# Optimization experiments

Hardware: AMD Instinct MI355X
Metric: run time of the kernel (lower is better)

## Reference

```python
import jax, jax.numpy as jnp
import numpy as np

B, T, C, H = 16, 2048, 1024, 64

def setup_inputs() -> dict:
    key = jax.random.key(0)
    kx, kq, kk, kv = jax.random.split(key, 4)
    s = 0.02
    return {
        "x": jax.random.normal(kx, (B, T, C), dtype=jnp.float32),
        "Wq": jax.random.normal(kq, (C, H), dtype=jnp.float32) * s,
        "Wk": jax.random.normal(kk, (C, H), dtype=jnp.float32) * s,
        "Wv": jax.random.normal(kv, (C, H), dtype=jnp.float32) * s,
    }

def reference(x, Wq, Wk, Wv):
    Bc, Tc, Cc = x.shape
    q = x @ Wq  # [B,T,H]
    k = x @ Wk  # [B,T,H]
    v = x @ Wv  # [B,T,H]
    # NOTE: original scales by n_embed^{-0.5} (C), not head_size^{-0.5}
    wei = jnp.einsum("bth,bsh->bts", q, k) * (Cc ** -0.5)  # [B,T,T]
    causal = jnp.tril(jnp.ones((Tc, Tc), dtype=bool))
    wei = jnp.where(causal, wei, -jnp.inf)
    wei = jax.nn.softmax(wei, axis=-1)
    # dropout is identity in eval mode
    out = jnp.einsum("bts,bsh->bth", wei, v)  # [B,T,H]
    return out
```

## Files before the change

### kernel.cpp

```cpp
#include <hip/hip_runtime.h>

typedef __attribute__((ext_vector_type(8))) short short8;
typedef __attribute__((ext_vector_type(4))) float float4v;

__device__ inline short f2bf(float f) {
    union { float f; unsigned int u; } c; c.f = f;
    unsigned int u = c.u;
    unsigned int r = (u + 0x7fffu + ((u >> 16) & 1u)) >> 16;
    return (short)r;
}

__device__ inline void gl2lds16(const short* g, short* l) {
    __builtin_amdgcn_global_load_lds(
        (const __attribute__((address_space(1))) unsigned int*)g,
        (__attribute__((address_space(3))) unsigned int*)l, 16, 0, 0);
}


__global__ __launch_bounds__(256) void wconv_kernel(
    const float* __restrict__ Wq, const float* __restrict__ Wk,
    const float* __restrict__ Wv, short* __restrict__ Wt_s)
{
    __shared__ short Ls[64 * 72];
    const int w  = blockIdx.x >> 4;
    const int c  = blockIdx.x & 15;
    const int k0 = c * 64;
    const float* W = (w == 0) ? Wq : (w == 1) ? Wk : Wv;
    const int tid = threadIdx.x;

#pragma unroll
    for (int i = 0; i < 4; i++) {
        int kk = (tid >> 4) + i * 16;
        int c4 = (tid & 15) * 4;
        float4 v = *(const float4*)&W[(size_t)(k0 + kk) * 64 + c4];
        Ls[kk * 72 + c4 + 0] = f2bf(v.x);
        Ls[kk * 72 + c4 + 1] = f2bf(v.y);
        Ls[kk * 72 + c4 + 2] = f2bf(v.z);
        Ls[kk * 72 + c4 + 3] = f2bf(v.w);
    }
    __syncthreads();
    const int n  = tid >> 2;
    const int k8 = (tid & 3) * 16;
    short8 o0, o1;
#pragma unroll
    for (int j = 0; j < 8; j++) o0[j] = Ls[(k8 + j) * 72 + n];
#pragma unroll
    for (int j = 0; j < 8; j++) o1[j] = Ls[(k8 + 8 + j) * 72 + n];
    const int gn = w * 64 + n;
    short* base = &Wt_s[((size_t)c * 192 + gn) * 64];
    int g0 = k8 >> 3;
    *(short8*)&base[((g0    ) ^ (gn & 7)) * 8] = o0;
    *(short8*)&base[((g0 + 1) ^ (gn & 7)) * 8] = o1;
}

__global__ __launch_bounds__(256) void qkv_kernel(
    const float* __restrict__ x, const short* __restrict__ Wt_s,
    short* __restrict__ qo, short* __restrict__ k_s, short* __restrict__ vT_t)
{
    __shared__ short As[32 * 72];
    __shared__ short Bs[192 * 64];

    const int tid  = threadIdx.x;
    const int wave = tid >> 6, lane = tid & 63;
    const int quad = lane >> 4, l16 = lane & 15;
    const int m0   = blockIdx.x * 32;

    float4v acc[2][3];
#pragma unroll
    for (int mf = 0; mf < 2; mf++)
#pragma unroll
        for (int nt = 0; nt < 3; nt++) acc[mf][nt] = (float4v)0.0f;

    const int arow = tid >> 3;
    const int acol = (tid & 7) * 8;
    const float* ap = &x[(size_t)(m0 + arow) * 1024 + acol];
    const int lofs = lane * 8;

    for (int kc = 0; kc < 1024; kc += 64) {
        __syncthreads();
        float4 x0 = *(const float4*)(ap + kc);
        float4 x1 = *(const float4*)(ap + kc + 4);
        short8 av;
        av[0]=f2bf(x0.x); av[1]=f2bf(x0.y); av[2]=f2bf(x0.z); av[3]=f2bf(x0.w);
        av[4]=f2bf(x1.x); av[5]=f2bf(x1.y); av[6]=f2bf(x1.z); av[7]=f2bf(x1.w);
        *(short8*)&As[arow * 72 + acol] = av;
        const short* gsrc = Wt_s + ((size_t)(kc >> 6) * 192 + wave * 48) * 64;
        short* ldst = &Bs[wave * 48 * 64];
#pragma unroll
        for (int i = 0; i < 6; i++)
            gl2lds16(gsrc + i * 512 + lofs, ldst + i * 512 + lofs);
        __syncthreads();
#pragma unroll
        for (int kc2 = 0; kc2 < 2; kc2++) {
            short8 a0 = *(const short8*)&As[(l16)      * 72 + kc2*32 + quad*8];
            short8 a1 = *(const short8*)&As[(16 + l16) * 72 + kc2*32 + quad*8];
#pragma unroll
            for (int nt = 0; nt < 3; nt++) {
                int brow = wave * 48 + nt * 16 + l16;
                int g = kc2 * 4 + quad;
                short8 bf = *(const short8*)&Bs[brow * 64 + (g ^ (brow & 7)) * 8];
                acc[0][nt] = __builtin_amdgcn_mfma_f32_16x16x32_bf16(a0, bf, acc[0][nt], 0, 0, 0);
                acc[1][nt] = __builtin_amdgcn_mfma_f32_16x16x32_bf16(a1, bf, acc[1][nt], 0, 0, 0);
            }
        }
    }
#pragma unroll
    for (int mf = 0; mf < 2; mf++) {
#pragma unroll
        for (int nt = 0; nt < 3; nt++) {
            int g = wave * 48 + nt * 16 + l16;
#pragma unroll
            for (int r = 0; r < 4; r++) {
                int row = m0 + mf * 16 + quad * 4 + r;
                short val = f2bf(acc[mf][nt][r]);
                if (g < 64) {
                    qo[(size_t)row * 64 + g] = val;
                } else if (g < 128) {
                    int h = g - 64;
                    k_s[(size_t)row * 64 + (((h >> 3) ^ (row & 7)) * 8 + (h & 7))] = val;
                } else {
                    int h = g - 128;
                    int bb = row >> 11, tt = row & 2047;
                    int tc = tt >> 6, tl = tt & 63;
                    vT_t[(((size_t)bb * 32 + tc) * 64 + h) * 64 +
                         (((tl >> 3) ^ (h & 7)) * 8 + (tl & 7))] = val;
                }
            }
        }
    }
}

#define SCALE_LOG2E 0.04508422132f

__global__ __launch_bounds__(128) void attn_kernel(
    const short* __restrict__ q, const short* __restrict__ k_s,
    const short* __restrict__ vT_t, float* __restrict__ out)
{
    __shared__ short Ks[64 * 64];
    __shared__ short Vs[64 * 64];
    __shared__ short Ps[32 * 72];

    const int tid  = threadIdx.x;
    const int wave = tid >> 6, lane = tid & 63;
    const int quad = lane >> 4, l16 = lane & 15;

    int b, qt;
    if (blockIdx.x < 512) { b = blockIdx.x >> 5; qt = 32 + (blockIdx.x & 31); }
    else { int t2 = blockIdx.x - 512; b = t2 >> 5; qt = 31 - (t2 & 31); }

    const short* kb = k_s  + (size_t)b * 2048 * 64;
    const short* vb = vT_t + (size_t)b * 32 * 64 * 64;

    const short* qrow = q + ((size_t)b * 2048 + qt*32 + wave*16 + l16) * 64;
    short8 qf0 = *(const short8*)&qrow[quad*8];
    short8 qf1 = *(const short8*)&qrow[32 + quad*8];

    float4v oacc[4];
#pragma unroll
    for (int t = 0; t < 4; t++) oacc[t] = (float4v)0.0f;
    float l_i[4] = {0.f, 0.f, 0.f, 0.f};

    const int tg   = qt*32 + wave*16 + quad*4;
    const int jmax = qt >> 1;
    const int lofs = lane * 8;

    for (int j = 0; j <= jmax; j++) {
        __syncthreads();
        const short* kg = kb + ((size_t)j * 64 + wave * 32) * 64;
        short* kl = &Ks[wave * 32 * 64];
#pragma unroll
        for (int i = 0; i < 4; i++)
            gl2lds16(kg + i * 512 + lofs, kl + i * 512 + lofs);
        const short* vg = vb + ((size_t)j * 64 + wave * 32) * 64;
        short* vl = &Vs[wave * 32 * 64];
#pragma unroll
        for (int i = 0; i < 4; i++)
            gl2lds16(vg + i * 512 + lofs, vl + i * 512 + lofs);
        __syncthreads();

        float4v sacc[4];
#pragma unroll
        for (int t = 0; t < 4; t++) sacc[t] = (float4v)0.0f;
#pragma unroll
        for (int t = 0; t < 4; t++) {
            int brow = t*16 + l16;
            short8 b0 = *(const short8*)&Ks[brow * 64 + ((    quad) ^ (brow & 7)) * 8];
            short8 b1 = *(const short8*)&Ks[brow * 64 + ((4 + quad) ^ (brow & 7)) * 8];
            sacc[t] = __builtin_amdgcn_mfma_f32_16x16x32_bf16(qf0, b0, sacc[t], 0, 0, 0);
            sacc[t] = __builtin_amdgcn_mfma_f32_16x16x32_bf16(qf1, b1, sacc[t], 0, 0, 0);
        }
        if (j == jmax) {
#pragma unroll
            for (int t = 0; t < 4; t++) {
                int sg = j*64 + t*16 + l16;
#pragma unroll
                for (int r = 0; r < 4; r++) {
                    float p = exp2f(sacc[t][r] * SCALE_LOG2E);
                    if (sg > tg + r) p = 0.0f;
                    sacc[t][r] = p;
                    l_i[r] += p;
                }
            }
        } else {
#pragma unroll
            for (int t = 0; t < 4; t++)
#pragma unroll
                for (int r = 0; r < 4; r++) {
                    float p = exp2f(sacc[t][r] * SCALE_LOG2E);
                    sacc[t][r] = p;
                    l_i[r] += p;
                }
        }
#pragma unroll
        for (int t = 0; t < 4; t++)
#pragma unroll
            for (int r = 0; r < 4; r++)
                Ps[(wave*16 + quad*4 + r) * 72 + t*16 + l16] = f2bf(sacc[t][r]);
#pragma unroll
        for (int kc = 0; kc < 2; kc++) {
            short8 af = *(const short8*)&Ps[(wave*16 + l16) * 72 + kc*32 + quad*8];
#pragma unroll
            for (int t = 0; t < 4; t++) {
                int drow = t*16 + l16;
                short8 bf = *(const short8*)&Vs[drow * 64 + ((kc*4 + quad) ^ (drow & 7)) * 8];
                oacc[t] = __builtin_amdgcn_mfma_f32_16x16x32_bf16(af, bf, oacc[t], 0, 0, 0);
            }
        }
    }
#pragma unroll
    for (int off = 1; off < 16; off <<= 1)
#pragma unroll
        for (int r = 0; r < 4; r++)
            l_i[r] += __shfl_xor(l_i[r], off, 64);
#pragma unroll
    for (int r = 0; r < 4; r++) {
        float inv = 1.0f / l_i[r];
        int row = qt*32 + wave*16 + quad*4 + r;
#pragma unroll
        for (int t = 0; t < 4; t++)
            out[((size_t)b * 2048 + row) * 64 + t*16 + l16] = oacc[t][r] * inv;
    }
}

extern "C" void kernel_launch(void* const* d_in, const int* in_sizes, int n_in,
                              void* d_out, int out_size, void* d_ws, size_t ws_size,
                              hipStream_t stream)
{
    const float* x  = (const float*)d_in[0];
    const float* Wq = (const float*)d_in[1];
    const float* Wk = (const float*)d_in[2];
    const float* Wv = (const float*)d_in[3];

    short* qw   = (short*)d_ws;
    short* ks   = qw + (size_t)32768 * 64;
    short* vTt  = ks + (size_t)32768 * 64;
    short* Wts  = vTt + (size_t)32768 * 64;
    float* out  = (float*)d_out;

    hipLaunchKernelGGL(wconv_kernel, dim3(48), dim3(256), 0, stream,
                       Wq, Wk, Wv, Wts);
    hipLaunchKernelGGL(qkv_kernel, dim3(1024), dim3(256), 0, stream,
                       x, Wts, qw, ks, vTt);
    hipLaunchKernelGGL(attn_kernel, dim3(1024), dim3(128), 0, stream,
                       qw, ks, vTt, out);
}
```

Before: 251.9 us.

## Software-pipeline QKV projection loads and widen attention KV tile to 128

The projection GEMM now prefetches the next x chunk and weight tile while running MFMAs on register-held fragments from the previous tile, so global loads overlap compute. The attention kernel processes 128 keys per iteration instead of 64, halving loop iterations and barriers per query tile. It also stores P in a swizzled 128-wide LDS layout to avoid bank conflicts. The cost is more registers and LDS per block, and more masked work on the diagonal tile, which can lower occupancy.

```diff
diff --git a/kernel.cpp b/kernel.cpp
--- a/kernel.cpp
+++ b/kernel.cpp
@@ -75,32 +75,72 @@
     const int acol = (tid & 7) * 8;
     const float* ap = &x[(size_t)(m0 + arow) * 1024 + acol];
     const int lofs = lane * 8;
+    short* bdst = &Bs[wave * 48 * 64];
+
+    short8 ra[2][2], rb[2][3];
+    float4 ax0, ax1;
+
+    ax0 = *(const float4*)(ap + 0);
+    ax1 = *(const float4*)(ap + 4);
+    {
+        const short* gs = Wt_s + ((size_t)0 * 192 + wave * 48) * 64;
+#pragma unroll
+        for (int i = 0; i < 6; i++)
+            gl2lds16(gs + i * 512 + lofs, bdst + i * 512 + lofs);
+    }
+    {
+        short8 av;
+        av[0]=f2bf(ax0.x); av[1]=f2bf(ax0.y); av[2]=f2bf(ax0.z); av[3]=f2bf(ax0.w);
+        av[4]=f2bf(ax1.x); av[5]=f2bf(ax1.y); av[6]=f2bf(ax1.z); av[7]=f2bf(ax1.w);
+        *(short8*)&As[arow * 72 + acol] = av;
+    }
+    __syncthreads();
+#pragma unroll
+    for (int kc2 = 0; kc2 < 2; kc2++) {
+        ra[kc2][0] = *(const short8*)&As[(l16)      * 72 + kc2*32 + quad*8];
+        ra[kc2][1] = *(const short8*)&As[(16 + l16) * 72 + kc2*32 + quad*8];
+#pragma unroll
+        for (int nt = 0; nt < 3; nt++) {
+            int brow = wave * 48 + nt * 16 + l16;
+            rb[kc2][nt] = *(const short8*)&Bs[brow * 64 + (((kc2*4 + quad)) ^ (brow & 7)) * 8];
+        }
+    }
 
     for (int kc = 0; kc < 1024; kc += 64) {
+        const bool notlast = (kc < 960);
         __syncthreads();
-        float4 x0 = *(const float4*)(ap + kc);
-        float4 x1 = *(const float4*)(ap + kc + 4);
-        short8 av;
-        av[0]=f2bf(x0.x); av[1]=f2bf(x0.y); av[2]=f2bf(x0.z); av[3]=f2bf(x0.w);
-        av[4]=f2bf(x1.x); av[5]=f2bf(x1.y); av[6]=f2bf(x1.z); av[7]=f2bf(x1.w);
-        *(short8*)&As[arow * 72 + acol] = av;
-        const short* gsrc = Wt_s + ((size_t)(kc >> 6) * 192 + wave * 48) * 64;
-        short* ldst = &Bs[wave * 48 * 64];
-#pragma unroll
-        for (int i = 0; i < 6; i++)
-            gl2lds16(gsrc + i * 512 + lofs, ldst + i * 512 + lofs);
+        if (notlast) {
+            ax0 = *(const float4*)(ap + kc + 64);
+            ax1 = *(const float4*)(ap + kc + 68);
+            const short* gs = Wt_s + ((size_t)((kc >> 6) + 1) * 192 + wave * 48) * 64;
+#pragma unroll
+            for (int i = 0; i < 6; i++)
+                gl2lds16(gs + i * 512 + lofs, bdst + i * 512 + lofs);
+        }
+#pragma unroll
+        for (int kc2 = 0; kc2 < 2; kc2++)
+#pragma unroll
+            for (int nt = 0; nt < 3; nt++) {
+                acc[0][nt] = __builtin_amdgcn_mfma_f32_16x16x32_bf16(ra[kc2][0], rb[kc2][nt], acc[0][nt], 0, 0, 0);
+                acc[1][nt] = __builtin_amdgcn_mfma_f32_16x16x32_bf16(ra[kc2][1], rb[kc2][nt], acc[1][nt], 0, 0, 0);
+            }
+        if (notlast) {
+            short8 av;
+            av[0]=f2bf(ax0.x); av[1]=f2bf(ax0.y); av[2]=f2bf(ax0.z); av[3]=f2bf(ax0.w);
+            av[4]=f2bf(ax1.x); av[5]=f2bf(ax1.y); av[6]=f2bf(ax1.z); av[7]=f2bf(ax1.w);
+            *(short8*)&As[arow * 72 + acol] = av;
+        }
         __syncthreads();
-#pragma unroll
-        for (int kc2 = 0; kc2 < 2; kc2++) {
-            short8 a0 = *(const short8*)&As[(l16)      * 72 + kc2*32 + quad*8];
-            short8 a1 = *(const short8*)&As[(16 + l16) * 72 + kc2*32 + quad*8];
-#pragma unroll
-            for (int nt = 0; nt < 3; nt++) {
-                int brow = wave * 48 + nt * 16 + l16;
-                int g = kc2 * 4 + quad;
-                short8 bf = *(const short8*)&Bs[brow * 64 + (g ^ (brow & 7)) * 8];
-                acc[0][nt] = __builtin_amdgcn_mfma_f32_16x16x32_bf16(a0, bf, acc[0][nt], 0, 0, 0);
-                acc[1][nt] = __builtin_amdgcn_mfma_f32_16x16x32_bf16(a1, bf, acc[1][nt], 0, 0, 0);
+        if (notlast) {
+#pragma unroll
+            for (int kc2 = 0; kc2 < 2; kc2++) {
+                ra[kc2][0] = *(const short8*)&As[(l16)      * 72 + kc2*32 + quad*8];
+                ra[kc2][1] = *(const short8*)&As[(16 + l16) * 72 + kc2*32 + quad*8];
+#pragma unroll
+                for (int nt = 0; nt < 3; nt++) {
+                    int brow = wave * 48 + nt * 16 + l16;
+                    rb[kc2][nt] = *(const short8*)&Bs[brow * 64 + (((kc2*4 + quad)) ^ (brow & 7)) * 8];
+                }
             }
         }
     }
@@ -136,9 +176,9 @@
     const short* __restrict__ q, const short* __restrict__ k_s,
     const short* __restrict__ vT_t, float* __restrict__ out)
 {
-    __shared__ short Ks[64 * 64];
-    __shared__ short Vs[64 * 64];
-    __shared__ short Ps[32 * 72];
+    __shared__ short Ks[128 * 64];
+    __shared__ short Vs[2 * 64 * 64];
+    __shared__ short Ps[32 * 128];
 
     const int tid  = threadIdx.x;
     const int wave = tid >> 6, lane = tid & 63;
@@ -161,28 +201,29 @@
     float l_i[4] = {0.f, 0.f, 0.f, 0.f};
 
     const int tg   = qt*32 + wave*16 + quad*4;
-    const int jmax = qt >> 1;
+    const int jmax = qt >> 2;
     const int lofs = lane * 8;
+    const int psw  = l16 & 7;
 
     for (int j = 0; j <= jmax; j++) {
         __syncthreads();
-        const short* kg = kb + ((size_t)j * 64 + wave * 32) * 64;
-        short* kl = &Ks[wave * 32 * 64];
-#pragma unroll
-        for (int i = 0; i < 4; i++)
+        const short* kg = kb + ((size_t)j * 128 + wave * 64) * 64;
+        short* kl = &Ks[wave * 64 * 64];
+#pragma unroll
+        for (int i = 0; i < 8; i++)
             gl2lds16(kg + i * 512 + lofs, kl + i * 512 + lofs);
-        const short* vg = vb + ((size_t)j * 64 + wave * 32) * 64;
-        short* vl = &Vs[wave * 32 * 64];
-#pragma unroll
-        for (int i = 0; i < 4; i++)
+        const short* vg = vb + (size_t)(2*j + wave) * 4096;
+        short* vl = &Vs[wave * 4096];
+#pragma unroll
+        for (int i = 0; i < 8; i++)
             gl2lds16(vg + i * 512 + lofs, vl + i * 512 + lofs);
         __syncthreads();
 
-        float4v sacc[4];
-#pragma unroll
-        for (int t = 0; t < 4; t++) sacc[t] = (float4v)0.0f;
-#pragma unroll
-        for (int t = 0; t < 4; t++) {
+        float4v sacc[8];
+#pragma unroll
+        for (int t = 0; t < 8; t++) sacc[t] = (float4v)0.0f;
+#pragma unroll
+        for (int t = 0; t < 8; t++) {
             int brow = t*16 + l16;
             short8 b0 = *(const short8*)&Ks[brow * 64 + ((    quad) ^ (brow & 7)) * 8];
             short8 b1 = *(const short8*)&Ks[brow * 64 + ((4 + quad) ^ (brow & 7)) * 8];
@@ -191,8 +232,8 @@
         }
         if (j == jmax) {
 #pragma unroll
-            for (int t = 0; t < 4; t++) {
-                int sg = j*64 + t*16 + l16;
+            for (int t = 0; t < 8; t++) {
+                int sg = j*128 + t*16 + l16;
 #pragma unroll
                 for (int r = 0; r < 4; r++) {
                     float p = exp2f(sacc[t][r] * SCALE_LOG2E);
@@ -203,7 +244,7 @@
             }
         } else {
 #pragma unroll
-            for (int t = 0; t < 4; t++)
+            for (int t = 0; t < 8; t++)
 #pragma unroll
                 for (int r = 0; r < 4; r++) {
                     float p = exp2f(sacc[t][r] * SCALE_LOG2E);
@@ -212,17 +253,21 @@
                 }
         }
 #pragma unroll
-        for (int t = 0; t < 4; t++)
-#pragma unroll
-            for (int r = 0; r < 4; r++)
-                Ps[(wave*16 + quad*4 + r) * 72 + t*16 + l16] = f2bf(sacc[t][r]);
-#pragma unroll
-        for (int kc = 0; kc < 2; kc++) {
-            short8 af = *(const short8*)&Ps[(wave*16 + l16) * 72 + kc*32 + quad*8];
+        for (int t = 0; t < 8; t++)
+#pragma unroll
+            for (int r = 0; r < 4; r++) {
+                int m = wave*16 + quad*4 + r;
+                int grp = (t*2 + (l16 >> 3)) ^ ((quad*4 + r) & 7);
+                Ps[m * 128 + grp * 8 + (l16 & 7)] = f2bf(sacc[t][r]);
+            }
+#pragma unroll
+        for (int kc = 0; kc < 4; kc++) {
+            short8 af = *(const short8*)&Ps[(wave*16 + l16) * 128 + ((kc*4 + quad) ^ psw) * 8];
 #pragma unroll
             for (int t = 0; t < 4; t++) {
                 int drow = t*16 + l16;
-                short8 bf = *(const short8*)&Vs[drow * 64 + ((kc*4 + quad) ^ (drow & 7)) * 8];
+                short8 bf = *(const short8*)&Vs[(kc >> 1) * 4096 + drow * 64 +
+                                                (((kc & 1)*4 + quad) ^ (drow & 7)) * 8];
                 oacc[t] = __builtin_amdgcn_mfma_f32_16x16x32_bf16(af, bf, oacc[t], 0, 0, 0);
             }
         }
```

After: 254.7 us. About the same (+1.1%).

## Software-pipeline QKV and attention loads through registers, use single-wave attention blocks

Applied to the files above, without the earlier changes.

The QKV projection now loads x directly into registers in MFMA fragment layout, skipping the A-tile LDS staging. It prefetches the next weight chunk via global-to-LDS and the next x chunk while the current MFMAs run, with explicit waitcnt instead of block barriers. Attention becomes one wave per 16-row query tile, so no __syncthreads are needed. It keeps K/V fragments in registers so the next tile's K/V load overlaps compute, and uses a cheaper round-to-nearest bf16 conversion. This trades more VGPRs and twice the blocks for latency hiding, and relies on correct waitcnt encodings for ordering.

```diff
diff --git a/kernel.cpp b/kernel.cpp
--- a/kernel.cpp
+++ b/kernel.cpp
@@ -9,12 +9,23 @@
     unsigned int r = (u + 0x7fffu + ((u >> 16) & 1u)) >> 16;
     return (short)r;
 }
+__device__ inline short f2bf_fast(float f) {
+    union { float f; unsigned int u; } c; c.f = f;
+    return (short)((c.u + 0x8000u) >> 16);
+}
+__device__ inline unsigned int pkbf(float a, float b) {
+    union { float f; unsigned int u; } ca, cb; ca.f = a; cb.f = b;
+    return ((cb.u + 0x8000u) & 0xFFFF0000u) | ((ca.u + 0x8000u) >> 16);
+}
 
 __device__ inline void gl2lds16(const short* g, short* l) {
     __builtin_amdgcn_global_load_lds(
         (const __attribute__((address_space(1))) unsigned int*)g,
         (__attribute__((address_space(3))) unsigned int*)l, 16, 0, 0);
 }
+
+#define WAIT_VM0   __builtin_amdgcn_s_waitcnt(0x0f70)
+#define WAIT_LGKM0 __builtin_amdgcn_s_waitcnt(0xc07f)
 
 
 __global__ __launch_bounds__(256) void wconv_kernel(
@@ -57,7 +68,6 @@
     const float* __restrict__ x, const short* __restrict__ Wt_s,
     short* __restrict__ qo, short* __restrict__ k_s, short* __restrict__ vT_t)
 {
-    __shared__ short As[32 * 72];
     __shared__ short Bs[192 * 64];
 
     const int tid  = threadIdx.x;
@@ -71,38 +81,74 @@
 #pragma unroll
         for (int nt = 0; nt < 3; nt++) acc[mf][nt] = (float4v)0.0f;
 
-    const int arow = tid >> 3;
-    const int acol = (tid & 7) * 8;
-    const float* ap = &x[(size_t)(m0 + arow) * 1024 + acol];
     const int lofs = lane * 8;
-
-    for (int kc = 0; kc < 1024; kc += 64) {
-        __syncthreads();
-        float4 x0 = *(const float4*)(ap + kc);
-        float4 x1 = *(const float4*)(ap + kc + 4);
-        short8 av;
-        av[0]=f2bf(x0.x); av[1]=f2bf(x0.y); av[2]=f2bf(x0.z); av[3]=f2bf(x0.w);
-        av[4]=f2bf(x1.x); av[5]=f2bf(x1.y); av[6]=f2bf(x1.z); av[7]=f2bf(x1.w);
-        *(short8*)&As[arow * 72 + acol] = av;
-        const short* gsrc = Wt_s + ((size_t)(kc >> 6) * 192 + wave * 48) * 64;
-        short* ldst = &Bs[wave * 48 * 64];
+    short* bslab = &Bs[wave * 48 * 64];
+    const float* abase = &x[(size_t)(m0 + l16) * 1024 + quad * 8];
+
+    float4 ax[8];
+    short8 ra[2][2];
+    short8 rb[2][3];
+
+    {
+        const short* gs = Wt_s + (size_t)(wave * 48) * 64;
 #pragma unroll
         for (int i = 0; i < 6; i++)
-            gl2lds16(gsrc + i * 512 + lofs, ldst + i * 512 + lofs);
-        __syncthreads();
+            gl2lds16(gs + i * 512 + lofs, bslab + i * 512 + lofs);
+    }
+#pragma unroll
+    for (int mf = 0; mf < 2; mf++)
 #pragma unroll
         for (int kc2 = 0; kc2 < 2; kc2++) {
-            short8 a0 = *(const short8*)&As[(l16)      * 72 + kc2*32 + quad*8];
-            short8 a1 = *(const short8*)&As[(16 + l16) * 72 + kc2*32 + quad*8];
+            const float* p = abase + mf * 16384 + kc2 * 32;
+            ax[mf*4 + kc2*2 + 0] = *(const float4*)p;
+            ax[mf*4 + kc2*2 + 1] = *(const float4*)(p + 4);
+        }
+
+    for (int c = 0; c < 16; c++) {
+#pragma unroll
+        for (int mf = 0; mf < 2; mf++)
+#pragma unroll
+            for (int kc2 = 0; kc2 < 2; kc2++) {
+                float4 x0 = ax[mf*4 + kc2*2 + 0];
+                float4 x1 = ax[mf*4 + kc2*2 + 1];
+                short8 a;
+                *((unsigned int*)&a + 0) = pkbf(x0.x, x0.y);
+                *((unsigned int*)&a + 1) = pkbf(x0.z, x0.w);
+                *((unsigned int*)&a + 2) = pkbf(x1.x, x1.y);
+                *((unsigned int*)&a + 3) = pkbf(x1.z, x1.w);
+                ra[kc2][mf] = a;
+            }
+        WAIT_VM0;
+#pragma unroll
+        for (int kc2 = 0; kc2 < 2; kc2++)
 #pragma unroll
             for (int nt = 0; nt < 3; nt++) {
                 int brow = wave * 48 + nt * 16 + l16;
-                int g = kc2 * 4 + quad;
-                short8 bf = *(const short8*)&Bs[brow * 64 + (g ^ (brow & 7)) * 8];
-                acc[0][nt] = __builtin_amdgcn_mfma_f32_16x16x32_bf16(a0, bf, acc[0][nt], 0, 0, 0);
-                acc[1][nt] = __builtin_amdgcn_mfma_f32_16x16x32_bf16(a1, bf, acc[1][nt], 0, 0, 0);
-            }
-        }
+                rb[kc2][nt] = *(const short8*)&Bs[brow * 64 + ((kc2*4 + quad) ^ (brow & 7)) * 8];
+            }
+        WAIT_LGKM0;
+        if (c < 15) {
+            const short* gs = Wt_s + ((size_t)(c + 1) * 192 + wave * 48) * 64;
+#pragma unroll
+            for (int i = 0; i < 6; i++)
+                gl2lds16(gs + i * 512 + lofs, bslab + i * 512 + lofs);
+            const float* an = abase + (c + 1) * 64;
+#pragma unroll
+            for (int mf = 0; mf < 2; mf++)
+#pragma unroll
+                for (int kc2 = 0; kc2 < 2; kc2++) {
+                    const float* p = an + mf * 16384 + kc2 * 32;
+                    ax[mf*4 + kc2*2 + 0] = *(const float4*)p;
+                    ax[mf*4 + kc2*2 + 1] = *(const float4*)(p + 4);
+                }
+        }
+#pragma unroll
+        for (int kc2 = 0; kc2 < 2; kc2++)
+#pragma unroll
+            for (int nt = 0; nt < 3; nt++) {
+                acc[0][nt] = __builtin_amdgcn_mfma_f32_16x16x32_bf16(ra[kc2][0], rb[kc2][nt], acc[0][nt], 0, 0, 0);
+                acc[1][nt] = __builtin_amdgcn_mfma_f32_16x16x32_bf16(ra[kc2][1], rb[kc2][nt], acc[1][nt], 0, 0, 0);
+            }
     }
 #pragma unroll
     for (int mf = 0; mf < 2; mf++) {
@@ -132,67 +178,74 @@
 
 #define SCALE_LOG2E 0.04508422132f
 
-__global__ __launch_bounds__(128) void attn_kernel(
+__global__ __launch_bounds__(64) void attn_kernel(
     const short* __restrict__ q, const short* __restrict__ k_s,
     const short* __restrict__ vT_t, float* __restrict__ out)
 {
     __shared__ short Ks[64 * 64];
     __shared__ short Vs[64 * 64];
-    __shared__ short Ps[32 * 72];
-
-    const int tid  = threadIdx.x;
-    const int wave = tid >> 6, lane = tid & 63;
+    __shared__ short Ps[16 * 72];
+
+    const int lane = threadIdx.x;
     const int quad = lane >> 4, l16 = lane & 15;
 
-    int b, qt;
-    if (blockIdx.x < 512) { b = blockIdx.x >> 5; qt = 32 + (blockIdx.x & 31); }
-    else { int t2 = blockIdx.x - 512; b = t2 >> 5; qt = 31 - (t2 & 31); }
+    const int b = blockIdx.x >> 7;
+    const int i = blockIdx.x & 127;
+    const int qt = (i & 1) ? (i >> 1) : (127 - (i >> 1));
 
     const short* kb = k_s  + (size_t)b * 2048 * 64;
     const short* vb = vT_t + (size_t)b * 32 * 64 * 64;
 
-    const short* qrow = q + ((size_t)b * 2048 + qt*32 + wave*16 + l16) * 64;
-    short8 qf0 = *(const short8*)&qrow[quad*8];
-    short8 qf1 = *(const short8*)&qrow[32 + quad*8];
+    const short* qrow = q + ((size_t)b * 2048 + qt * 16 + l16) * 64;
+    short8 qf0 = *(const short8*)&qrow[quad * 8];
+    short8 qf1 = *(const short8*)&qrow[32 + quad * 8];
 
     float4v oacc[4];
 #pragma unroll
     for (int t = 0; t < 4; t++) oacc[t] = (float4v)0.0f;
     float l_i[4] = {0.f, 0.f, 0.f, 0.f};
 
-    const int tg   = qt*32 + wave*16 + quad*4;
-    const int jmax = qt >> 1;
+    const int tg   = qt * 16 + quad * 4;
+    const int jmax = qt >> 2;
     const int lofs = lane * 8;
 
+#pragma unroll
+    for (int s = 0; s < 8; s++) gl2lds16(kb + s * 512 + lofs, Ks + s * 512 + lofs);
+#pragma unroll
+    for (int s = 0; s < 8; s++) gl2lds16(vb + s * 512 + lofs, Vs + s * 512 + lofs);
+
     for (int j = 0; j <= jmax; j++) {
-        __syncthreads();
-        const short* kg = kb + ((size_t)j * 64 + wave * 32) * 64;
-        short* kl = &Ks[wave * 32 * 64];
-#pragma unroll
-        for (int i = 0; i < 4; i++)
-            gl2lds16(kg + i * 512 + lofs, kl + i * 512 + lofs);
-        const short* vg = vb + ((size_t)j * 64 + wave * 32) * 64;
-        short* vl = &Vs[wave * 32 * 64];
-#pragma unroll
-        for (int i = 0; i < 4; i++)
-            gl2lds16(vg + i * 512 + lofs, vl + i * 512 + lofs);
-        __syncthreads();
-
+        WAIT_VM0;
+        short8 kf[4][2], vf[4][2];
+#pragma unroll
+        for (int t = 0; t < 4; t++) {
+            int br = t * 16 + l16;
+            kf[t][0] = *(const short8*)&Ks[br * 64 + (((    quad)) ^ (br & 7)) * 8];
+            kf[t][1] = *(const short8*)&Ks[br * 64 + (((4 + quad)) ^ (br & 7)) * 8];
+            vf[t][0] = *(const short8*)&Vs[br * 64 + (((    quad)) ^ (br & 7)) * 8];
+            vf[t][1] = *(const short8*)&Vs[br * 64 + (((4 + quad)) ^ (br & 7)) * 8];
+        }
+        WAIT_LGKM0;
+        if (j < jmax) {
+            const short* kg = kb + (size_t)(j + 1) * 4096;
+            const short* vg = vb + (size_t)(j + 1) * 4096;
+#pragma unroll
+            for (int s = 0; s < 8; s++) gl2lds16(kg + s * 512 + lofs, Ks + s * 512 + lofs);
+#pragma unroll
+            for (int s = 0; s < 8; s++) gl2lds16(vg + s * 512 + lofs, Vs + s * 512 + lofs);
+        }
         float4v sacc[4];
 #pragma unroll
         for (int t = 0; t < 4; t++) sacc[t] = (float4v)0.0f;
 #pragma unroll
         for (int t = 0; t < 4; t++) {
-            int brow = t*16 + l16;
-            short8 b0 = *(const short8*)&Ks[brow * 64 + ((    quad) ^ (brow & 7)) * 8];
-            short8 b1 = *(const short8*)&Ks[brow * 64 + ((4 + quad) ^ (brow & 7)) * 8];
-            sacc[t] = __builtin_amdgcn_mfma_f32_16x16x32_bf16(qf0, b0, sacc[t], 0, 0, 0);
-            sacc[t] = __builtin_amdgcn_mfma_f32_16x16x32_bf16(qf1, b1, sacc[t], 0, 0, 0);
+            sacc[t] = __builtin_amdgcn_mfma_f32_16x16x32_bf16(qf0, kf[t][0], sacc[t], 0, 0, 0);
+            sacc[t] = __builtin_amdgcn_mfma_f32_16x16x32_bf16(qf1, kf[t][1], sacc[t], 0, 0, 0);
         }
         if (j == jmax) {
 #pragma unroll
             for (int t = 0; t < 4; t++) {
-                int sg = j*64 + t*16 + l16;
+                int sg = j * 64 + t * 16 + l16;
 #pragma unroll
                 for (int r = 0; r < 4; r++) {
                     float p = exp2f(sacc[t][r] * SCALE_LOG2E);
@@ -215,16 +268,13 @@
         for (int t = 0; t < 4; t++)
 #pragma unroll
             for (int r = 0; r < 4; r++)
-                Ps[(wave*16 + quad*4 + r) * 72 + t*16 + l16] = f2bf(sacc[t][r]);
+                Ps[(quad * 4 + r) * 72 + t * 16 + l16] = f2bf_fast(sacc[t][r]);
 #pragma unroll
         for (int kc = 0; kc < 2; kc++) {
-            short8 af = *(const short8*)&Ps[(wave*16 + l16) * 72 + kc*32 + quad*8];
-#pragma unroll
-            for (int t = 0; t < 4; t++) {
-                int drow = t*16 + l16;
-                short8 bf = *(const short8*)&Vs[drow * 64 + ((kc*4 + quad) ^ (drow & 7)) * 8];
-                oacc[t] = __builtin_amdgcn_mfma_f32_16x16x32_bf16(af, bf, oacc[t], 0, 0, 0);
-            }
+            short8 af = *(const short8*)&Ps[l16 * 72 + kc * 32 + quad * 8];
+#pragma unroll
+            for (int t = 0; t < 4; t++)
+                oacc[t] = __builtin_amdgcn_mfma_f32_16x16x32_bf16(af, vf[t][kc], oacc[t], 0, 0, 0);
         }
     }
 #pragma unroll
@@ -235,10 +285,10 @@
 #pragma unroll
     for (int r = 0; r < 4; r++) {
         float inv = 1.0f / l_i[r];
-        int row = qt*32 + wave*16 + quad*4 + r;
+        int row = qt * 16 + quad * 4 + r;
 #pragma unroll
         for (int t = 0; t < 4; t++)
-            out[((size_t)b * 2048 + row) * 64 + t*16 + l16] = oacc[t][r] * inv;
+            out[((size_t)b * 2048 + row) * 64 + t * 16 + l16] = oacc[t][r] * inv;
     }
 }
 
@@ -261,6 +311,6 @@
                        Wq, Wk, Wv, Wts);
     hipLaunchKernelGGL(qkv_kernel, dim3(1024), dim3(256), 0, stream,
                        x, Wts, qw, ks, vTt);
-    hipLaunchKernelGGL(attn_kernel, dim3(1024), dim3(128), 0, stream,
+    hipLaunchKernelGGL(attn_kernel, dim3(2048), dim3(64), 0, stream,
                        qw, ks, vTt, out);
 }
```

After: 291.5 us. 15.7% more time.
